# Optimization experiments

Measured on AMD Instinct MI355X. Metric: run time of the kernel, lower is better.

Reference implementation:

```python
import jax, jax.numpy as jnp
import numpy as np


def setup_inputs() -> dict:
    key = jax.random.key(0)
    ks = jax.random.split(key, 5)
    B, S, E, H, D = 4, 2048, 1024, 16, 64
    sc = 1.0 / np.sqrt(E)
    x = jax.random.normal(ks[0], (B, S, E), dtype=jnp.float32)
    Wq = jax.random.normal(ks[1], (H, E, D), dtype=jnp.float32) * sc
    Wk = jax.random.normal(ks[2], (H, E, D), dtype=jnp.float32) * sc
    Wv = jax.random.normal(ks[3], (H, E, D), dtype=jnp.float32) * sc
    Wo = jax.random.normal(ks[4], (E, E), dtype=jnp.float32) * sc
    bo = jnp.zeros((E,), dtype=jnp.float32)
    return {"x": x, "Wq": Wq, "Wk": Wk, "Wv": Wv, "Wo": Wo, "bo": bo}


def reference(x, Wq, Wk, Wv, Wo, bo):
    # x: [B,S,E]; Wq/Wk/Wv: [H,E,D]; Wo: [E,E]; bo: [E]
    B, S, E = x.shape
    H, _, D = Wq.shape
    q = jnp.einsum('bse,hed->bhsd', x, Wq)
    k = jnp.einsum('bse,hed->bhsd', x, Wk)
    v = jnp.einsum('bse,hed->bhsd', x, Wv)
    scale = jnp.asarray(D, x.dtype) ** -0.5
    att = jnp.einsum('bhsd,bhtd->bhst', q, k) * scale  # [B,H,S,S]
    causal = jnp.tril(jnp.ones((S, S), dtype=bool))
    att = jnp.where(causal, att, jnp.asarray(-jnp.inf, att.dtype))
    att = jax.nn.softmax(att, axis=-1)
    out = jnp.einsum('bhst,bhtd->bhsd', att, v)  # [B,H,S,D]
    # concat heads in order (head dim-major on last axis), then project
    out = out.transpose(0, 2, 1, 3).reshape(B, S, H * D)
    return out @ Wo.T + bo
```

## Files before the change

kernel.cpp:

```cpp
#include <hip/hip_runtime.h>
#include <hip/hip_bf16.h>

#define BB 4
#define SS 2048
#define EE 1024
#define HH 16
#define DD 64
#define MM (BB*SS)
#define HD (HH*DD)
#define NQKV (3*HD)

typedef __bf16 bf16_t;
typedef __bf16 bf16x4 __attribute__((ext_vector_type(4)));
typedef __bf16 bf16x8 __attribute__((ext_vector_type(8)));
typedef float f32x4 __attribute__((ext_vector_type(4)));

#define MFMA16(a,b,c) __builtin_amdgcn_mfma_f32_16x16x32_bf16(a,b,c,0,0,0)
#define NEG_INF (-__builtin_huge_valf())
#define QSCALE 0.1803368801111204f
#define CSHIFT 12.0f

__device__ __forceinline__ void gload_lds16(const void* g, void* l) {
  __builtin_amdgcn_global_load_lds((const __attribute__((address_space(1))) unsigned int*)g,
                                   (__attribute__((address_space(3))) unsigned int*)l,
                                   16, 0, 0);
}

#define SBAR() __builtin_amdgcn_s_barrier()
#define SCHB() __builtin_amdgcn_sched_barrier(0)
#define VMCNT2 do { asm volatile("s_waitcnt vmcnt(2)" ::: "memory"); } while(0)
#define VMCNT0 do { asm volatile("s_waitcnt vmcnt(0)" ::: "memory"); } while(0)

__global__ __launch_bounds__(256)
void k_f32_to_bf16(const float* __restrict__ in, bf16_t* __restrict__ out, int n8) {
  int i = blockIdx.x*256 + threadIdx.x;
  if (i >= n8) return;
  const float4* p = reinterpret_cast<const float4*>(in) + (size_t)i*2;
  float4 a = p[0], b = p[1];
  bf16x8 o;
  o[0]=(bf16_t)a.x; o[1]=(bf16_t)a.y; o[2]=(bf16_t)a.z; o[3]=(bf16_t)a.w;
  o[4]=(bf16_t)b.x; o[5]=(bf16_t)b.y; o[6]=(bf16_t)b.z; o[7]=(bf16_t)b.w;
  *reinterpret_cast<bf16x8*>(out + (size_t)i*8) = o;
}

__global__ __launch_bounds__(256)
void k_conv_wqkv(const float* __restrict__ Wq, const float* __restrict__ Wk,
                 const float* __restrict__ Wv, bf16_t* __restrict__ Wt) {
  __shared__ float t[64][65];
  int wh = blockIdx.x;
  int which = wh >> 4, h = wh & 15;
  int e0 = blockIdx.y * 64;
  const float* W = (which==0) ? Wq : (which==1) ? Wk : Wv;
  const float* src = W + (size_t)h*EE*DD;
  int r = threadIdx.x >> 6, c = threadIdx.x & 63;
  #pragma unroll
  for (int i = 0; i < 16; ++i) {
    int e = i*4 + r;
    t[e][c] = src[(size_t)(e0+e)*DD + c];
  }
  __syncthreads();
  bf16_t* dst = Wt + (size_t)(which*HD + h*DD)*EE;
  #pragma unroll
  for (int i = 0; i < 16; ++i) {
    int d = i*4 + r;
    dst[(size_t)d*EE + e0 + c] = (bf16_t)t[c][d];
  }
}

#define QK_ITERS 8
template<int EPI, int NTX>
__global__ __launch_bounds__(512, 1)
void k_gemm8(const bf16_t* __restrict__ Ag, const bf16_t* __restrict__ Bg0,
             bf16_t* __restrict__ Qp, bf16_t* __restrict__ Kp, bf16_t* __restrict__ Vtp,
             const float* __restrict__ bias, float* __restrict__ Cout) {
  __shared__ __align__(16) bf16_t Ab[2][128*64];
  __shared__ __align__(16) bf16_t Bb[2][256*64];

  int orig = blockIdx.x;
  int xcd = orig & 7, lidx = orig >> 3;
  int tileY = xcd*8 + (lidx & 7);
  int tileX = lidx >> 3;
  int n0 = tileX * 256, m0 = tileY * 128;

  int tid = threadIdx.x;
  int lane = tid & 63, w = tid >> 6;
  int wr = w >> 2, wc = w & 3;
  int lr = lane & 15, lg = lane >> 4;

  const bf16_t* Bg = Bg0 + (size_t)n0 * EE;

  int r3 = tid >> 3;
  int gch = (tid & 7) ^ (r3 & 7);
  int ldsb = w * 1024;

#define STAGE_A(buf, kt) do { \
    const bf16_t* g_ = Ag + (size_t)(m0 + r3)*EE + (kt)*64 + gch*8; \
    char* l_ = (char*)Ab[buf] + ldsb; \
    gload_lds16(g_, l_); \
    gload_lds16(g_ + (size_t)64*EE, l_ + 8192); \
  } while(0)
#define STAGE_B(buf, kt, half) do { \
    const bf16_t* g_ = Bg + (size_t)((half)*128 + r3)*EE + (kt)*64 + gch*8; \
    char* l_ = (char*)Bb[buf] + (half)*16384 + ldsb; \
    gload_lds16(g_, l_); \
    gload_lds16(g_ + (size_t)64*EE, l_ + 8192); \
  } while(0)

  int sA = lr & 7;
  unsigned aoff[2] = { (unsigned)((wr*64 + lr)*128 + ((lg     ^ sA) << 4)),
                       (unsigned)((wr*64 + lr)*128 + (((4+lg) ^ sA) << 4)) };
  unsigned boff[2] = { (unsigned)((wc*64 + lr)*128 + ((lg     ^ sA) << 4)),
                       (unsigned)((wc*64 + lr)*128 + (((4+lg) ^ sA) << 4)) };

  f32x4 acc[4][4];
  #pragma unroll
  for (int i=0;i<4;i++)
    #pragma unroll
    for (int j=0;j<4;j++) acc[i][j] = (f32x4){0.f,0.f,0.f,0.f};
  bf16x8 af[4], b0, b1;

#define PHASE(buf, kh, nh, WAITV, ...) do { \
    if ((nh) == 0) { \
      _Pragma("unroll") for (int mf_=0; mf_<4; ++mf_) \
        af[mf_] = *reinterpret_cast<const bf16x8*>((const char*)Ab[buf] + aoff[kh] + mf_*2048); \
    } \
    b0 = *reinterpret_cast<const bf16x8*>((const char*)Bb[buf] + boff[kh] + (nh)*4096); \
    b1 = *reinterpret_cast<const bf16x8*>((const char*)Bb[buf] + boff[kh] + (nh)*4096 + 2048); \
    __VA_ARGS__; \
    SBAR(); \
    asm volatile("s_waitcnt lgkmcnt(0)" ::: "memory"); \
    SCHB(); \
    __builtin_amdgcn_s_setprio(1); \
    _Pragma("unroll") for (int mf_=0; mf_<4; ++mf_) { \
      acc[mf_][(nh)*2+0] = MFMA16(af[mf_], b0, acc[mf_][(nh)*2+0]); \
      acc[mf_][(nh)*2+1] = MFMA16(af[mf_], b1, acc[mf_][(nh)*2+1]); } \
    __builtin_amdgcn_s_setprio(0); \
    WAITV; \
    SBAR(); \
    SCHB(); \
  } while(0)

  STAGE_A(0, 0);
  STAGE_B(0, 0, 0); STAGE_B(0, 0, 1);
  STAGE_A(1, 1);
  VMCNT2;
  SBAR();
  SCHB();

#define WAITQ { if (!last) { VMCNT2; } else { VMCNT0; } }
  for (int i = 0; i < QK_ITERS; ++i) {
    int t1 = 2*i+1, t2 = 2*i+2, t3 = 2*i+3;
    bool last = (i == QK_ITERS-1);
    PHASE(0, 0, 0, (void)0, STAGE_B(1, t1, 0));
    PHASE(0, 0, 1, (void)0, STAGE_B(1, t1, 1));
    PHASE(0, 1, 0, (void)0, (void)0);
    PHASE(0, 1, 1, WAITQ,   if (!last) STAGE_A(0, t2));
    PHASE(1, 0, 0, (void)0, if (!last) STAGE_B(0, t2, 0));
    PHASE(1, 0, 1, (void)0, if (!last) STAGE_B(0, t2, 1));
    PHASE(1, 1, 0, (void)0, (void)0);
    PHASE(1, 1, 1, WAITQ,   if (!last) STAGE_A(1, t3));
  }
#undef WAITQ
#undef PHASE
#undef STAGE_A
#undef STAGE_B

  if (EPI == 0) {
    int which = n0 >> 10;
    if (which < 2) {
      #pragma unroll
      for (int mf=0; mf<4; ++mf) {
        #pragma unroll
        for (int nf=0; nf<4; ++nf) {
          int n = n0 + wc*64 + nf*16 + lr;
          int hd = n & 1023, h2 = hd >> 6, d = hd & 63;
          #pragma unroll
          for (int r=0;r<4;r++) {
            int m = m0 + wr*64 + mf*16 + lg*4 + r;
            int b = m >> 11, s = m & 2047;
            size_t bh = (size_t)(b*HH + h2);
            if (which == 0) Qp[(bh*SS + s)*DD + d] = (bf16_t)(acc[mf][nf][r] * QSCALE);
            else            Kp[(bh*SS + s)*DD + d] = (bf16_t)acc[mf][nf][r];
          }
        }
      }
    } else {
      #pragma unroll
      for (int mf=0; mf<4; ++mf) {
        #pragma unroll
        for (int nf=0; nf<4; ++nf) {
          int n = n0 + wc*64 + nf*16 + lr;
          int hd = n & 1023, h2 = hd >> 6, d = hd & 63;
          int m = m0 + wr*64 + mf*16 + lg*4;
          int b = m >> 11, s = m & 2047;
          size_t bh = (size_t)(b*HH + h2);
          bf16x4 vv;
          vv[0] = (bf16_t)acc[mf][nf][0];
          vv[1] = (bf16_t)acc[mf][nf][1];
          vv[2] = (bf16_t)acc[mf][nf][2];
          vv[3] = (bf16_t)acc[mf][nf][3];
          *reinterpret_cast<bf16x4*>(Vtp + (bh*DD + d)*SS + s) = vv;
        }
      }
    }
  } else {
    float bv[4];
    #pragma unroll
    for (int nf=0;nf<4;nf++) bv[nf] = bias[n0 + wc*64 + nf*16 + lr];
    #pragma unroll
    for (int mf=0; mf<4; ++mf)
      #pragma unroll
      for (int nf=0; nf<4; ++nf) {
        int n = n0 + wc*64 + nf*16 + lr;
        #pragma unroll
        for (int r=0;r<4;r++) {
          int m = m0 + wr*64 + mf*16 + lg*4 + r;
          Cout[(size_t)m*HD + n] = acc[mf][nf][r] + bv[nf];
        }
      }
  }
}

__global__ __launch_bounds__(512)
void k_attn(const bf16_t* __restrict__ Q, const bf16_t* __restrict__ K,
            const bf16_t* __restrict__ Vt, bf16_t* __restrict__ AO) {
  __shared__ __align__(16) bf16_t Ks[3][64*64];
  __shared__ __align__(16) bf16_t Vs[3][64*64];

  int id = blockIdx.x;
  int m8 = id & 7, d8 = id >> 3;
  int bh = m8*8 + (d8 >> 3);
  int u  = d8 & 7;

  int tid = threadIdx.x, lane = tid & 63, w = tid >> 6;
  int lr = lane & 15, lg = lane >> 4;
  const bf16_t* Qb = Q  + (size_t)bh * SS * DD;
  const bf16_t* Kp = K  + (size_t)bh * SS * DD;
  const bf16_t* Vp = Vt + (size_t)bh * DD * SS;
  int b = bh >> 4, h = bh & 15;

  int srow = tid >> 3;
  int gchunk = (tid & 7) ^ (srow & 7);

  bf16x8 onesf;
  #pragma unroll
  for (int i=0;i<8;i++) onesf[i] = (bf16_t)1.0f;

#define STAGE_KV(t, buf) do { \
    int kv0_ = (t)*64; \
    gload_lds16(Kp + (size_t)(kv0_ + srow)*DD + gchunk*8, (char*)Ks[buf] + w*1024); \
    gload_lds16(Vp + (size_t)srow*SS + kv0_ + gchunk*8,   (char*)Vs[buf] + w*1024); \
  } while(0)

  for (int ph = 0; ph < 2; ++ph) {
    int p = ph ? (15 - u) : u;
    int nt = 2*p + 2;
    int qrow0 = p*128 + w*16;
    int q = qrow0 + lr;

    bf16x8 qf[2];
    #pragma unroll
    for (int kk=0;kk<2;kk++)
      qf[kk] = *reinterpret_cast<const bf16x8*>(Qb + (size_t)(qrow0 + lr)*DD + kk*32 + lg*8);

    f32x4 po[4];
    #pragma unroll
    for (int i=0;i<4;i++) po[i] = (f32x4){0.f,0.f,0.f,0.f};
    f32x4 acclv = (f32x4){0.f,0.f,0.f,0.f};

    STAGE_KV(0, 0);
    STAGE_KV(1, 1);
    for (int t = 0; t < nt; ++t) {
      if (t < nt-1) { VMCNT2; } else { VMCNT0; }
      SBAR();
      SCHB();
      if (t+2 < nt) STAGE_KV(t+2, (t+2)%3);
      int kv0 = t*64;
      if (kv0 > qrow0 + 15) continue;
      int buf = t % 3;
      const bf16_t* Kb = Ks[buf];
      const bf16_t* Vb = Vs[buf];

      f32x4 sa[4];
      #pragma unroll
      for (int ct=0; ct<4; ++ct) {
        int rr = ct*16 + lr;
        int sw = rr & 7;
        bf16x8 k0 = *reinterpret_cast<const bf16x8*>(Kb + rr*64 + ((lg     ^ sw) << 3));
        bf16x8 k1 = *reinterpret_cast<const bf16x8*>(Kb + rr*64 + (((4+lg) ^ sw) << 3));
        f32x4 c = (f32x4){0.f,0.f,0.f,0.f};
        c = MFMA16(k0, qf[0], c);
        c = MFMA16(k1, qf[1], c);
        sa[ct] = c;
      }
      if (kv0 + 63 > qrow0) {
        #pragma unroll
        for (int ct=0;ct<4;ct++) {
          #pragma unroll
          for (int r=0;r<4;r++) {
            int kv = kv0 + ct*16 + lg*4 + r;
            if (kv > q) sa[ct][r] = NEG_INF;
          }
        }
      }
      bf16x8 pf[2];
      #pragma unroll
      for (int ct=0;ct<4;ct++)
        #pragma unroll
        for (int r=0;r<4;r++)
          pf[ct>>1][(ct&1)*4 + r] = (bf16_t)__builtin_amdgcn_exp2f(sa[ct][r] - CSHIFT);
      acclv = MFMA16(onesf, pf[0], acclv);
      acclv = MFMA16(onesf, pf[1], acclv);
      #pragma unroll
      for (int ctd=0; ctd<4; ++ctd) {
        int rr = ctd*16 + lr;
        int sw8 = rr & 7;
        int sub = (lg & 1) << 3;
        const char* rowb = (const char*)Vb + rr*128;
        #pragma unroll
        for (int kk=0; kk<2; ++kk) {
          int c0 = kk*4 + (lg>>1);
          bf16x4 lo = *reinterpret_cast<const bf16x4*>(rowb + (((c0     ^ sw8) << 4) | sub));
          bf16x4 hi = *reinterpret_cast<const bf16x4*>(rowb + ((((c0+2) ^ sw8) << 4) | sub));
          bf16x8 vf;
          vf[0]=lo[0]; vf[1]=lo[1]; vf[2]=lo[2]; vf[3]=lo[3];
          vf[4]=hi[0]; vf[5]=hi[1]; vf[6]=hi[2]; vf[7]=hi[3];
          po[ctd] = MFMA16(vf, pf[kk], po[ctd]);
        }
      }
    }
    SBAR();
    {
      float inv = 1.0f / acclv[0];
      bf16_t* dst = AO + (size_t)(b*SS + q)*HD + h*DD;
      #pragma unroll
      for (int ctd=0;ctd<4;ctd++) {
        bf16x4 vv;
        #pragma unroll
        for (int r=0;r<4;r++) vv[r] = (bf16_t)(po[ctd][r] * inv);
        *reinterpret_cast<bf16x4*>(dst + ctd*16 + lg*4) = vv;
      }
    }
  }
#undef STAGE_KV
}

extern "C" void kernel_launch(void* const* d_in, const int* in_sizes, int n_in,
                              void* d_out, int out_size, void* d_ws, size_t ws_size,
                              hipStream_t stream) {
  const float* x  = (const float*)d_in[0];
  const float* Wq = (const float*)d_in[1];
  const float* Wk = (const float*)d_in[2];
  const float* Wv = (const float*)d_in[3];
  const float* Wo = (const float*)d_in[4];
  const float* bo = (const float*)d_in[5];
  float* out = (float*)d_out;

  char* ws = (char*)d_ws;
  bf16_t* xb  = (bf16_t*)(ws + 0);
  bf16_t* wt  = (bf16_t*)(ws + 16777216);
  bf16_t* wob = (bf16_t*)(ws + 23068672);
  bf16_t* Qb  = (bf16_t*)(ws + 25165824);
  bf16_t* Kb  = (bf16_t*)(ws + 41943040);
  bf16_t* Vtb = (bf16_t*)(ws + 58720256);
  bf16_t* AO  = (bf16_t*)(ws + 75497472);

  k_f32_to_bf16<<<(MM*EE/8)/256, 256, 0, stream>>>(x,  xb,  MM*EE/8);
  k_f32_to_bf16<<<(EE*EE/8)/256, 256, 0, stream>>>(Wo, wob, EE*EE/8);
  dim3 gw(48, 16);
  k_conv_wqkv<<<gw, 256, 0, stream>>>(Wq, Wk, Wv, wt);

  k_gemm8<0,12><<<768, 512, 0, stream>>>(xb, wt, Qb, Kb, Vtb, nullptr, nullptr);

  k_attn<<<BB*HH*8, 512, 0, stream>>>(Qb, Kb, Vtb, AO);

  k_gemm8<1,4><<<256, 512, 0, stream>>>(AO, wob, nullptr, nullptr, nullptr, bo, out);
}
```

Baseline: 172.5 us.

## Use 128-wide KV tiles with double buffering in attention kernel

Doubles the KV tile processed per loop iteration from 64 to 128 keys and switches from a triple buffer to a double buffer in LDS, with a barrier after the compute before the next tile is staged. The aim is to halve the number of iterations and barriers and to give each wave more MFMA work between synchronizations. In exchange, LDS per block grows from 48KB to 64KB, which may lower occupancy. The per-wave skip of fully masked tiles is gone, so on the diagonal tile waves compute masked scores that were skipped before.

```diff
diff --git a/kernel.cpp b/kernel.cpp
--- a/kernel.cpp
+++ b/kernel.cpp
@@ -28,6 +28,7 @@
 
 #define SBAR() __builtin_amdgcn_s_barrier()
 #define SCHB() __builtin_amdgcn_sched_barrier(0)
+#define VMCNT4 do { asm volatile("s_waitcnt vmcnt(4)" ::: "memory"); } while(0)
 #define VMCNT2 do { asm volatile("s_waitcnt vmcnt(2)" ::: "memory"); } while(0)
 #define VMCNT0 do { asm volatile("s_waitcnt vmcnt(0)" ::: "memory"); } while(0)
 
@@ -224,8 +225,8 @@
 __global__ __launch_bounds__(512)
 void k_attn(const bf16_t* __restrict__ Q, const bf16_t* __restrict__ K,
             const bf16_t* __restrict__ Vt, bf16_t* __restrict__ AO) {
-  __shared__ __align__(16) bf16_t Ks[3][64*64];
-  __shared__ __align__(16) bf16_t Vs[3][64*64];
+  __shared__ __align__(16) bf16_t Ks[2][128*64];
+  __shared__ __align__(16) bf16_t Vs[2][64*128];
 
   int id = blockIdx.x;
   int m8 = id & 7, d8 = id >> 3;
@@ -239,22 +240,28 @@
   const bf16_t* Vp = Vt + (size_t)bh * DD * SS;
   int b = bh >> 4, h = bh & 15;
 
-  int srow = tid >> 3;
-  int gchunk = (tid & 7) ^ (srow & 7);
+  int krow = tid >> 3;
+  int kch  = (tid & 7) ^ (krow & 7);
+  int vrow = tid >> 4;
+  int vch  = (tid & 15) ^ (vrow & 15);
 
   bf16x8 onesf;
   #pragma unroll
   for (int i=0;i<8;i++) onesf[i] = (bf16_t)1.0f;
 
 #define STAGE_KV(t, buf) do { \
-    int kv0_ = (t)*64; \
-    gload_lds16(Kp + (size_t)(kv0_ + srow)*DD + gchunk*8, (char*)Ks[buf] + w*1024); \
-    gload_lds16(Vp + (size_t)srow*SS + kv0_ + gchunk*8,   (char*)Vs[buf] + w*1024); \
+    int kv0_ = (t)*128; \
+    const bf16_t* kg_ = Kp + (size_t)(kv0_ + krow)*DD + kch*8; \
+    gload_lds16(kg_,                 (char*)Ks[buf] + w*1024); \
+    gload_lds16(kg_ + (size_t)64*DD, (char*)Ks[buf] + 8192 + w*1024); \
+    const bf16_t* vg_ = Vp + (size_t)vrow*SS + kv0_ + vch*8; \
+    gload_lds16(vg_,                 (char*)Vs[buf] + w*1024); \
+    gload_lds16(vg_ + (size_t)32*SS, (char*)Vs[buf] + 8192 + w*1024); \
   } while(0)
 
   for (int ph = 0; ph < 2; ++ph) {
     int p = ph ? (15 - u) : u;
-    int nt = 2*p + 2;
+    int nt = p + 1;
     int qrow0 = p*128 + w*16;
     int q = qrow0 + lr;
 
@@ -271,65 +278,69 @@
     STAGE_KV(0, 0);
     STAGE_KV(1, 1);
     for (int t = 0; t < nt; ++t) {
-      if (t < nt-1) { VMCNT2; } else { VMCNT0; }
+      if (t < nt-1) { VMCNT4; } else { VMCNT0; }
       SBAR();
       SCHB();
-      if (t+2 < nt) STAGE_KV(t+2, (t+2)%3);
-      int kv0 = t*64;
-      if (kv0 > qrow0 + 15) continue;
-      int buf = t % 3;
-      const bf16_t* Kb = Ks[buf];
-      const bf16_t* Vb = Vs[buf];
-
-      f32x4 sa[4];
-      #pragma unroll
-      for (int ct=0; ct<4; ++ct) {
-        int rr = ct*16 + lr;
-        int sw = rr & 7;
-        bf16x8 k0 = *reinterpret_cast<const bf16x8*>(Kb + rr*64 + ((lg     ^ sw) << 3));
-        bf16x8 k1 = *reinterpret_cast<const bf16x8*>(Kb + rr*64 + (((4+lg) ^ sw) << 3));
-        f32x4 c = (f32x4){0.f,0.f,0.f,0.f};
-        c = MFMA16(k0, qf[0], c);
-        c = MFMA16(k1, qf[1], c);
-        sa[ct] = c;
-      }
-      if (kv0 + 63 > qrow0) {
-        #pragma unroll
-        for (int ct=0;ct<4;ct++) {
+      int kv0 = t*128;
+      const bf16_t* Kb = Ks[t&1];
+      const bf16_t* Vb = Vs[t&1];
+      bool diag = (t == nt-1);
+
+      bf16x8 pf[4];
+      #pragma unroll
+      for (int kh=0; kh<2; ++kh) {
+        f32x4 sa[4];
+        #pragma unroll
+        for (int c4=0; c4<4; ++c4) {
+          int rr = (kh*4 + c4)*16 + lr;
+          int sw = rr & 7;
+          bf16x8 k0 = *reinterpret_cast<const bf16x8*>(Kb + rr*64 + ((lg     ^ sw) << 3));
+          bf16x8 k1 = *reinterpret_cast<const bf16x8*>(Kb + rr*64 + (((4+lg) ^ sw) << 3));
+          f32x4 c = (f32x4){0.f,0.f,0.f,0.f};
+          c = MFMA16(k0, qf[0], c);
+          c = MFMA16(k1, qf[1], c);
+          sa[c4] = c;
+        }
+        if (diag) {
           #pragma unroll
-          for (int r=0;r<4;r++) {
-            int kv = kv0 + ct*16 + lg*4 + r;
-            if (kv > q) sa[ct][r] = NEG_INF;
-          }
-        }
-      }
-      bf16x8 pf[2];
-      #pragma unroll
-      for (int ct=0;ct<4;ct++)
-        #pragma unroll
-        for (int r=0;r<4;r++)
-          pf[ct>>1][(ct&1)*4 + r] = (bf16_t)__builtin_amdgcn_exp2f(sa[ct][r] - CSHIFT);
+          for (int c4=0;c4<4;c4++)
+            #pragma unroll
+            for (int r=0;r<4;r++) {
+              int kv = kv0 + (kh*4+c4)*16 + lg*4 + r;
+              if (kv > q) sa[c4][r] = NEG_INF;
+            }
+        }
+        #pragma unroll
+        for (int c4=0;c4<4;c4++)
+          #pragma unroll
+          for (int r=0;r<4;r++)
+            pf[kh*2 + (c4>>1)][(c4&1)*4 + r] =
+                (bf16_t)__builtin_amdgcn_exp2f(sa[c4][r] - CSHIFT);
+      }
       acclv = MFMA16(onesf, pf[0], acclv);
       acclv = MFMA16(onesf, pf[1], acclv);
+      acclv = MFMA16(onesf, pf[2], acclv);
+      acclv = MFMA16(onesf, pf[3], acclv);
       #pragma unroll
       for (int ctd=0; ctd<4; ++ctd) {
         int rr = ctd*16 + lr;
-        int sw8 = rr & 7;
+        int sw16 = rr & 15;
         int sub = (lg & 1) << 3;
-        const char* rowb = (const char*)Vb + rr*128;
-        #pragma unroll
-        for (int kk=0; kk<2; ++kk) {
+        const char* rowb = (const char*)Vb + rr*256;
+        #pragma unroll
+        for (int kk=0; kk<4; ++kk) {
           int c0 = kk*4 + (lg>>1);
-          bf16x4 lo = *reinterpret_cast<const bf16x4*>(rowb + (((c0     ^ sw8) << 4) | sub));
-          bf16x4 hi = *reinterpret_cast<const bf16x4*>(rowb + ((((c0+2) ^ sw8) << 4) | sub));
+          bf16x4 lo = *reinterpret_cast<const bf16x4*>(rowb + (((c0     ^ sw16) << 4) | sub));
+          bf16x4 hi = *reinterpret_cast<const bf16x4*>(rowb + ((((c0+2) ^ sw16) << 4) | sub));
           bf16x8 vf;
           vf[0]=lo[0]; vf[1]=lo[1]; vf[2]=lo[2]; vf[3]=lo[3];
           vf[4]=hi[0]; vf[5]=hi[1]; vf[6]=hi[2]; vf[7]=hi[3];
           po[ctd] = MFMA16(vf, pf[kk], po[ctd]);
         }
       }
+      SBAR();
+      if (t+2 < nt) STAGE_KV(t+2, t&1);
     }
-    SBAR();
     {
       float inv = 1.0f / acclv[0];
       bf16_t* dst = AO + (size_t)(b*SS + q)*HD + h*DD;
```

Result: slower. 186.4 us (+8.0%).

## Triple-buffer GEMM LDS pipeline with prefetch distance two and wider phases

Applied to the files above, without the earlier changes.

Moves the projection GEMM from a double-buffered LDS scheme to a three-buffer ring that prefetches K-tile t+2 while tile t is computed. Each phase now covers a full k-half with 16 MFMAs, so there are half as many barriers per tile. The goal is to hide global-to-LDS latency and cut sync overhead. In exchange LDS use grows to 144KB and the vmcnt bookkeeping gets more fragile.

```diff
diff --git a/kernel.cpp b/kernel.cpp
--- a/kernel.cpp
+++ b/kernel.cpp
@@ -28,6 +28,7 @@
 
 #define SBAR() __builtin_amdgcn_s_barrier()
 #define SCHB() __builtin_amdgcn_sched_barrier(0)
+#define VMCNT6 do { asm volatile("s_waitcnt vmcnt(6)" ::: "memory"); } while(0)
 #define VMCNT2 do { asm volatile("s_waitcnt vmcnt(2)" ::: "memory"); } while(0)
 #define VMCNT0 do { asm volatile("s_waitcnt vmcnt(0)" ::: "memory"); } while(0)
 
@@ -67,14 +68,14 @@
   }
 }
 
-#define QK_ITERS 8
+#define NKT 16
 template<int EPI, int NTX>
 __global__ __launch_bounds__(512, 1)
 void k_gemm8(const bf16_t* __restrict__ Ag, const bf16_t* __restrict__ Bg0,
              bf16_t* __restrict__ Qp, bf16_t* __restrict__ Kp, bf16_t* __restrict__ Vtp,
              const float* __restrict__ bias, float* __restrict__ Cout) {
-  __shared__ __align__(16) bf16_t Ab[2][128*64];
-  __shared__ __align__(16) bf16_t Bb[2][256*64];
+  __shared__ __align__(16) bf16_t Ab[3][128*64];
+  __shared__ __align__(16) bf16_t Bb[3][256*64];
 
   int orig = blockIdx.x;
   int xcd = orig & 7, lidx = orig >> 3;
@@ -117,51 +118,42 @@
   for (int i=0;i<4;i++)
     #pragma unroll
     for (int j=0;j<4;j++) acc[i][j] = (f32x4){0.f,0.f,0.f,0.f};
-  bf16x8 af[4], b0, b1;
-
-#define PHASE(buf, kh, nh, WAITV, ...) do { \
-    if ((nh) == 0) { \
-      _Pragma("unroll") for (int mf_=0; mf_<4; ++mf_) \
-        af[mf_] = *reinterpret_cast<const bf16x8*>((const char*)Ab[buf] + aoff[kh] + mf_*2048); \
-    } \
-    b0 = *reinterpret_cast<const bf16x8*>((const char*)Bb[buf] + boff[kh] + (nh)*4096); \
-    b1 = *reinterpret_cast<const bf16x8*>((const char*)Bb[buf] + boff[kh] + (nh)*4096 + 2048); \
-    __VA_ARGS__; \
+  bf16x8 af[4], bq[4];
+
+#define PHASE2(buf, kh, STAGE_STMT, WAITV) do { \
+    _Pragma("unroll") for (int mf_=0; mf_<4; ++mf_) \
+      af[mf_] = *reinterpret_cast<const bf16x8*>((const char*)Ab[buf] + aoff[kh] + mf_*2048); \
+    _Pragma("unroll") for (int nf_=0; nf_<4; ++nf_) \
+      bq[nf_] = *reinterpret_cast<const bf16x8*>((const char*)Bb[buf] + boff[kh] + nf_*2048); \
+    STAGE_STMT; \
     SBAR(); \
     asm volatile("s_waitcnt lgkmcnt(0)" ::: "memory"); \
     SCHB(); \
     __builtin_amdgcn_s_setprio(1); \
-    _Pragma("unroll") for (int mf_=0; mf_<4; ++mf_) { \
-      acc[mf_][(nh)*2+0] = MFMA16(af[mf_], b0, acc[mf_][(nh)*2+0]); \
-      acc[mf_][(nh)*2+1] = MFMA16(af[mf_], b1, acc[mf_][(nh)*2+1]); } \
+    _Pragma("unroll") for (int mf_=0; mf_<4; ++mf_) \
+      _Pragma("unroll") for (int nf_=0; nf_<4; ++nf_) \
+        acc[mf_][nf_] = MFMA16(af[mf_], bq[nf_], acc[mf_][nf_]); \
     __builtin_amdgcn_s_setprio(0); \
     WAITV; \
     SBAR(); \
     SCHB(); \
   } while(0)
 
-  STAGE_A(0, 0);
-  STAGE_B(0, 0, 0); STAGE_B(0, 0, 1);
-  STAGE_A(1, 1);
-  VMCNT2;
+  STAGE_A(0, 0); STAGE_B(0, 0, 0); STAGE_B(0, 0, 1);
+  STAGE_A(1, 1); STAGE_B(1, 1, 0); STAGE_B(1, 1, 1);
+  VMCNT6;
   SBAR();
   SCHB();
 
-#define WAITQ { if (!last) { VMCNT2; } else { VMCNT0; } }
-  for (int i = 0; i < QK_ITERS; ++i) {
-    int t1 = 2*i+1, t2 = 2*i+2, t3 = 2*i+3;
-    bool last = (i == QK_ITERS-1);
-    PHASE(0, 0, 0, (void)0, STAGE_B(1, t1, 0));
-    PHASE(0, 0, 1, (void)0, STAGE_B(1, t1, 1));
-    PHASE(0, 1, 0, (void)0, (void)0);
-    PHASE(0, 1, 1, WAITQ,   if (!last) STAGE_A(0, t2));
-    PHASE(1, 0, 0, (void)0, if (!last) STAGE_B(0, t2, 0));
-    PHASE(1, 0, 1, (void)0, if (!last) STAGE_B(0, t2, 1));
-    PHASE(1, 1, 0, (void)0, (void)0);
-    PHASE(1, 1, 1, WAITQ,   if (!last) STAGE_A(1, t3));
-  }
-#undef WAITQ
-#undef PHASE
+  #pragma unroll
+  for (int t = 0; t < NKT; ++t) {
+    int cur = t % 3, pre = (t+2) % 3;
+    bool more = (t+2 < NKT);
+    PHASE2(cur, 0, if (more) STAGE_A(pre, t+2), (void)0);
+    PHASE2(cur, 1, if (more) { STAGE_B(pre, t+2, 0); STAGE_B(pre, t+2, 1); },
+           { if (more) { VMCNT6; } else { VMCNT0; } });
+  }
+#undef PHASE2
 #undef STAGE_A
 #undef STAGE_B
 
```

Result: faster. 162.5 us (-5.8%).
